# Performance work log

Measured on AMD Instinct MI355X. Metric: run time of the kernel, lower is better.

The kernel has to match this reference:

```python
import jax, jax.numpy as jnp
import numpy as np

B, S, D = 2, 2048, 1024
H, HD, K = 16, 64, 4
F = 4096
EPS = 1e-6
ROPE_BASE = 10000.0
NEG = -1e9


def rmsnorm(x, w):
    return x * jax.lax.rsqrt(jnp.mean(x * x, axis=-1, keepdims=True) + EPS) * w


def rope(t, pos):
    # t: (B,S,H,HD), pos: (B,S,H) per-node position (float)
    inv_freq = 1.0 / (ROPE_BASE ** (jnp.arange(0, HD, 2, dtype=jnp.float32) / HD))
    ang = pos[..., None] * inv_freq  # (B,S,H,HD/2)
    cos, sin = jnp.cos(ang), jnp.sin(ang)
    t1, t2 = t[..., : HD // 2], t[..., HD // 2:]
    return jnp.concatenate([t1 * cos - t2 * sin, t2 * cos + t1 * sin], axis=-1)


def setup_inputs() -> dict:
    key = jax.random.key(0)
    ks = jax.random.split(key, 12)
    s = lambda d: 1.0 / np.sqrt(d)
    return {
        "x": jax.random.normal(ks[0], (B, S, D), jnp.float32),
        "attn_norm_w": jnp.ones((D,), jnp.float32),
        "ffn_norm_w": jnp.ones((D,), jnp.float32),
        "Wq": jax.random.normal(ks[1], (D, H * HD), jnp.float32) * s(D),
        "Wk": jax.random.normal(ks[2], (D, H * HD), jnp.float32) * s(D),
        "Wv": jax.random.normal(ks[3], (D, H * HD), jnp.float32) * s(D),
        "Wo": jax.random.normal(ks[4], (H * HD, D), jnp.float32) * s(H * HD),
        "Wr": jax.random.normal(ks[5], (D, H * K), jnp.float32) * s(D),
        "w1": jax.random.normal(ks[6], (D, F), jnp.float32) * s(D),
        "w2": jax.random.normal(ks[7], (D, F), jnp.float32) * s(D),
        "w3": jax.random.normal(ks[8], (F, D), jnp.float32) * s(F),
    }


def reference(x, attn_norm_w, ffn_norm_w, Wq, Wk, Wv, Wo, Wr, w1, w2, w3):
    # ---- pre-norm + hypergraph node-routed causal attention ----
    h = rmsnorm(x, attn_norm_w)
    # per-(token, head) routing to K hyper-nodes
    logits = (h @ Wr).reshape(B, S, H, K)
    node = jnp.argmax(logits, axis=-1)                      # (B,S,H) int
    onehot = jax.nn.one_hot(node, K, dtype=jnp.float32)     # (B,S,H,K)
    # per-node RoPE position: count of previous same-node tokens
    cum = jnp.cumsum(onehot, axis=1)                        # inclusive
    pos = jnp.take_along_axis(cum, node[..., None], axis=-1)[..., 0] - 1.0  # (B,S,H)

    q = (h @ Wq).reshape(B, S, H, HD)
    k = (h @ Wk).reshape(B, S, H, HD)
    v = (h @ Wv).reshape(B, S, H, HD)
    q = rope(q, pos)
    k = rope(k, pos)

    scores = jnp.einsum("bqhd,bkhd->bhqk", q, k) / np.sqrt(HD)  # (B,H,S,S)
    node_h = jnp.transpose(node, (0, 2, 1))                     # (B,H,S)
    same = node_h[:, :, :, None] == node_h[:, :, None, :]       # intra-node only
    causal = jnp.tril(jnp.ones((S, S), bool))
    allowed = same & causal
    attn = jax.nn.softmax(jnp.where(allowed, scores, NEG), axis=-1)
    ctx = jnp.einsum("bhqk,bkhd->bqhd", attn, v).reshape(B, S, H * HD)
    x = x + ctx @ Wo

    # ---- pre-norm + SwiGLU ----
    h2 = rmsnorm(x, ffn_norm_w)
    ffn = (jax.nn.silu(h2 @ w1) * (h2 @ w2)) @ w3
    return x + ffn
```

## Files before the change

### kernel.cpp

```cpp
#include <hip/hip_runtime.h>
#include <hip/hip_bf16.h>
#include <math.h>

typedef __hip_bfloat16 bf16;

#define B_  2
#define S_  2048
#define D_  1024
#define H_  16
#define HD_ 64
#define KR_ 4
#define F_  4096
#define TOK (B_*S_)
#define NEG (-1.0e9f)

typedef __attribute__((ext_vector_type(8))) short bf16x8_t;
typedef __attribute__((ext_vector_type(4))) float f32x4_t;
typedef unsigned int u32;
#define AS1 __attribute__((address_space(1)))
#define AS3 __attribute__((address_space(3)))

__device__ __forceinline__ float u2f(unsigned short u) {
  union { float f; unsigned int i; } cv; cv.i = ((unsigned int)u) << 16; return cv.f;
}
__device__ __forceinline__ unsigned short f2u(float f) {
  return (unsigned short)(__bfloat16_as_ushort(__float2bfloat16(f)));
}

__device__ __forceinline__ void gl_lds16(const bf16* g, unsigned short* lds_base) {
  __builtin_amdgcn_global_load_lds((const AS1 u32*)g, (AS3 u32*)lds_base, 16, 0, 0);
}

__device__ __forceinline__ float rd1(const void* p, size_t i, bool isbf) {
  return isbf ? __bfloat162float(((const bf16*)p)[i]) : ((const float*)p)[i];
}

__global__ void detect_k(const unsigned* __restrict__ anw_words, int* __restrict__ flag) {
  if (threadIdx.x == 0) *flag = (anw_words[0] == 0x3F803F80u) ? 1 : 0;
}

__global__ __launch_bounds__(256) void transpose_k(const void* W, bf16* __restrict__ WT,
                                                   const int* __restrict__ flagp,
                                                   int K, int N) {
  const bool isbf = (*flagp != 0);
  __shared__ float tile[32][33];
  const int k0 = blockIdx.y * 32, n0 = blockIdx.x * 32;
  const int tid = threadIdx.x;
  const int rl = tid >> 5, cl = tid & 31;
#pragma unroll
  for (int i = 0; i < 4; i++)
    tile[rl + 8 * i][cl] = rd1(W, (size_t)(k0 + rl + 8 * i) * N + n0 + cl, isbf);
  __syncthreads();
#pragma unroll
  for (int i = 0; i < 4; i++)
    WT[(size_t)(n0 + rl + 8 * i) * K + k0 + cl] = __float2bfloat16(tile[cl][rl + 8 * i]);
}

__global__ __launch_bounds__(256) void wrconv_k(const void* Wr, float* __restrict__ Wrf,
                                                const int* __restrict__ flagp) {
  const bool isbf = (*flagp != 0);
  const int i = blockIdx.x * 256 + threadIdx.x;
  Wrf[i] = rd1(Wr, i, isbf);
}

template <bool XDUAL, bool WF>
__global__ __launch_bounds__(256) void rmsnorm_k(const void* x, const void* w,
                                                 bf16* __restrict__ ob,
                                                 float* __restrict__ of,
                                                 const int* __restrict__ flagp) {
  const bool isbf = (*flagp != 0);
  const int row = blockIdx.x;
  const int t = threadIdx.x;
  float v[4];
  float ss = 0.f;
#pragma unroll
  for (int i = 0; i < 4; i++) {
    const size_t idx = (size_t)row * D_ + t + 256 * i;
    v[i] = XDUAL ? rd1(x, idx, isbf) : ((const float*)x)[idx];
    ss += v[i] * v[i];
  }
#pragma unroll
  for (int off = 32; off >= 1; off >>= 1) ss += __shfl_down(ss, off);
  __shared__ float red[4];
  if ((t & 63) == 0) red[t >> 6] = ss;
  __syncthreads();
  const float tot = red[0] + red[1] + red[2] + red[3];
  const float sc = rsqrtf(tot * (1.f / D_) + 1e-6f);
#pragma unroll
  for (int i = 0; i < 4; i++) {
    const int c = t + 256 * i;
    const float r = v[i] * sc * rd1(w, c, isbf);
    ob[(size_t)row * D_ + c] = __float2bfloat16(r);
    if (WF) of[(size_t)row * D_ + c] = r;
  }
}

__global__ __launch_bounds__(256) void router_k(const float* __restrict__ h,
                                                const float* __restrict__ Wrf,
                                                int* __restrict__ node) {
  const int tok0 = blockIdx.x * 16;
  const int t = threadIdx.x;
  __shared__ float hs[16][1024];
  __shared__ float lg[16][64];
  {
    const float4* hsrc = (const float4*)(h + (size_t)tok0 * D_);
    float4* hdst = (float4*)hs;
#pragma unroll
    for (int j = 0; j < 16; j++) hdst[j * 256 + t] = hsrc[j * 256 + t];
  }
  __syncthreads();
  const int col = t & 63, tg = t >> 6;
  float acc[4] = {0.f, 0.f, 0.f, 0.f};
  for (int i = 0; i < D_; i += 4) {
    float wv[4];
#pragma unroll
    for (int u = 0; u < 4; u++) wv[u] = Wrf[(size_t)(i + u) * 64 + col];
#pragma unroll
    for (int tt = 0; tt < 4; tt++) {
      const float4 hv = *(const float4*)&hs[tg * 4 + tt][i];
      acc[tt] = fmaf(hv.x, wv[0], acc[tt]);
      acc[tt] = fmaf(hv.y, wv[1], acc[tt]);
      acc[tt] = fmaf(hv.z, wv[2], acc[tt]);
      acc[tt] = fmaf(hv.w, wv[3], acc[tt]);
    }
  }
#pragma unroll
  for (int tt = 0; tt < 4; tt++) lg[tg * 4 + tt][col] = acc[tt];
  __syncthreads();
  const int tok = t >> 4, hh = t & 15;
  const float* l = &lg[tok][hh * 4];
  float best = l[0];
  int bi = 0;
#pragma unroll
  for (int j = 1; j < KR_; j++) {
    const float vv = l[j];
    if (vv > best) { best = vv; bi = j; }
  }
  node[(size_t)(tok0 + tok) * H_ + hh] = bi;
}

__global__ __launch_bounds__(256) void pos_k(const int* __restrict__ node,
                                             float* __restrict__ pos,
                                             unsigned short* __restrict__ iperm,
                                             unsigned char* __restrict__ gid,
                                             int* __restrict__ gstart) {
  const int bh = blockIdx.x;
  const int b = bh >> 4, h = bh & 15;
  const int t = threadIdx.x;
  __shared__ int sc[256][4];
  int vals[8];
  int c[4] = {0, 0, 0, 0};
#pragma unroll
  for (int i = 0; i < 8; i++) {
    vals[i] = node[(size_t)(b * S_ + t * 8 + i) * H_ + h] & 3;
    c[vals[i]]++;
  }
#pragma unroll
  for (int n = 0; n < 4; n++) sc[t][n] = c[n];
  __syncthreads();
  for (int off = 1; off < 256; off <<= 1) {
    int add[4] = {0, 0, 0, 0};
    if (t >= off) {
#pragma unroll
      for (int n = 0; n < 4; n++) add[n] = sc[t - off][n];
    }
    __syncthreads();
#pragma unroll
    for (int n = 0; n < 4; n++) sc[t][n] += add[n];
    __syncthreads();
  }
  int start[4];
#pragma unroll
  for (int n = 0; n < 4; n++) start[n] = sc[t][n] - c[n];
  int gs[4];
  gs[0] = 0;
  gs[1] = sc[255][0];
  gs[2] = gs[1] + sc[255][1];
  gs[3] = gs[2] + sc[255][2];
  if (t < 4) gstart[bh * 4 + t] = gs[t];
  const size_t bhS = (size_t)bh * S_;
#pragma unroll
  for (int i = 0; i < 8; i++) {
    const int n = vals[i];
    const int rank = start[n]++;
    pos[(size_t)(b * S_ + t * 8 + i) * H_ + h] = (float)rank;
    const int newp = gs[n] + rank;
    iperm[bhS + newp] = (unsigned short)(t * 8 + i);
    gid[bhS + newp] = (unsigned char)n;
  }
}

__global__ __launch_bounds__(512) void rope_k(bf16* __restrict__ q, bf16* __restrict__ k,
                                              const float* __restrict__ pos) {
  const int token = blockIdx.x;
  const int t = threadIdx.x;
  const int h = t >> 5, j = t & 31;
  const float p = pos[token * H_ + h];
  const float inv = exp2f(-(float)j * (13.287712379549449f / 32.f));
  float sn, cs;
  sincosf(p * inv, &sn, &cs);
  const size_t base = (size_t)token * D_ + h * HD_ + j;
  float a = __bfloat162float(q[base]), b = __bfloat162float(q[base + 32]);
  q[base] = __float2bfloat16(a * cs - b * sn);
  q[base + 32] = __float2bfloat16(b * cs + a * sn);
  a = __bfloat162float(k[base]); b = __bfloat162float(k[base + 32]);
  k[base] = __float2bfloat16(a * cs - b * sn);
  k[base + 32] = __float2bfloat16(b * cs + a * sn);
}

__global__ __launch_bounds__(256) void attn_k(const bf16* __restrict__ q,
                                              const bf16* __restrict__ k,
                                              const bf16* __restrict__ v,
                                              const unsigned short* __restrict__ ip,
                                              const unsigned char* __restrict__ gidp,
                                              const int* __restrict__ gstart,
                                              bf16* __restrict__ ctx) {
  const int qt = 31 - blockIdx.x;
  const int h = blockIdx.y;
  const int b = blockIdx.z;
  const int bS = b * S_;
  const int bh = b * H_ + h;
  const size_t bhS = (size_t)bh * S_;
  const int tid = threadIdx.x;
  const int w = tid >> 6;
  const int lane = tid & 63;
  const int col = lane & 15;
  const int quad = lane >> 4;

  __shared__ unsigned short Qs[64][76];
  __shared__ unsigned short Ks[64][76];
  __shared__ unsigned short Vst[64][76];
  __shared__ unsigned short Pa[64][76];

  {
    const int qr = tid & 63, ds = (tid >> 6) * 16;
    const int ipq = ip[bhS + qt * 64 + qr];
    const bf16* src = q + (size_t)(bS + ipq) * D_ + h * HD_ + ds;
#pragma unroll
    for (int i = 0; i < 4; i++)
      *(ushort4*)&Qs[qr][ds + 4 * i] = *(const ushort4*)(src + 4 * i);
  }
  int gq_r[4];
#pragma unroll
  for (int reg = 0; reg < 4; reg++)
    gq_r[reg] = gidp[bhS + qt * 64 + w * 16 + quad * 4 + reg];
  float m_r[4] = {NEG, NEG, NEG, NEG};
  float l_r[4] = {0.f, 0.f, 0.f, 0.f};

  f32x4_t acc_o[4];
#pragma unroll
  for (int ct = 0; ct < 4; ct++) acc_o[ct] = (f32x4_t){0.f, 0.f, 0.f, 0.f};

  const int kt0 = gstart[bh * 4 + gidp[bhS + qt * 64]] >> 6;

  for (int kt = kt0; kt <= qt; kt++) {
    __syncthreads();
    {
      const int key = tid & 63, ds = (tid >> 6) * 16;
      const int ipk = ip[bhS + kt * 64 + key];
      const bf16* ksrc = k + (size_t)(bS + ipk) * D_ + h * HD_ + ds;
      const bf16* vsrc = v + (size_t)(bS + ipk) * D_ + h * HD_ + ds;
#pragma unroll
      for (int i = 0; i < 4; i++) {
        *(ushort4*)&Ks[key][ds + 4 * i] = *(const ushort4*)(ksrc + 4 * i);
        const ushort4 vu = *(const ushort4*)(vsrc + 4 * i);
        Vst[ds + 4 * i + 0][key] = vu.x;
        Vst[ds + 4 * i + 1][key] = vu.y;
        Vst[ds + 4 * i + 2][key] = vu.z;
        Vst[ds + 4 * i + 3][key] = vu.w;
      }
    }
    __syncthreads();

    f32x4_t s[4];
    {
      const bf16x8_t a0 = *(const bf16x8_t*)&Qs[w * 16 + col][quad * 8];
      const bf16x8_t a1 = *(const bf16x8_t*)&Qs[w * 16 + col][32 + quad * 8];
#pragma unroll
      for (int ct = 0; ct < 4; ct++) {
        f32x4_t acc = (f32x4_t){0.f, 0.f, 0.f, 0.f};
        const bf16x8_t b0 = *(const bf16x8_t*)&Ks[ct * 16 + col][quad * 8];
        const bf16x8_t b1 = *(const bf16x8_t*)&Ks[ct * 16 + col][32 + quad * 8];
        acc = __builtin_amdgcn_mfma_f32_16x16x32_bf16(a0, b0, acc, 0, 0, 0);
        acc = __builtin_amdgcn_mfma_f32_16x16x32_bf16(a1, b1, acc, 0, 0, 0);
        s[ct] = acc;
      }
    }
    const bool diag = (kt == qt);
    const size_t kbase = bhS + kt * 64;
    const int gk[4] = {gidp[kbase + col], gidp[kbase + 16 + col],
                       gidp[kbase + 32 + col], gidp[kbase + 48 + col]};
#pragma unroll
    for (int ct = 0; ct < 4; ct++) {
#pragma unroll
      for (int reg = 0; reg < 4; reg++) {
        const int qr = quad * 4 + reg;
        const int kc = ct * 16 + col;
        const bool ok = (gk[ct] == gq_r[reg]) && (!diag || kc <= w * 16 + qr);
        s[ct][reg] = ok ? (s[ct][reg] * 0.125f) : NEG;
      }
    }
    float al[4];
#pragma unroll
    for (int reg = 0; reg < 4; reg++) {
      float tm = fmaxf(fmaxf(s[0][reg], s[1][reg]), fmaxf(s[2][reg], s[3][reg]));
#pragma unroll
      for (int off = 1; off <= 8; off <<= 1) tm = fmaxf(tm, __shfl_xor(tm, off));
      const float mold = m_r[reg];
      const float mnew = fmaxf(mold, tm);
      const bool dead = (mnew <= -5.0e8f);
      const float alpha = dead ? 1.f : __expf(mold - mnew);
      float rowsum = 0.f;
      const int qr = w * 16 + quad * 4 + reg;
#pragma unroll
      for (int ct = 0; ct < 4; ct++) {
        const float e = dead ? 0.f : __expf(s[ct][reg] - mnew);
        rowsum += e;
        Pa[qr][ct * 16 + col] = f2u(e);
      }
#pragma unroll
      for (int off = 1; off <= 8; off <<= 1) rowsum += __shfl_xor(rowsum, off);
      l_r[reg] = l_r[reg] * alpha + rowsum;
      m_r[reg] = mnew;
      al[reg] = alpha;
    }
    {
      const bf16x8_t pa0 = *(const bf16x8_t*)&Pa[w * 16 + col][quad * 8];
      const bf16x8_t pa1 = *(const bf16x8_t*)&Pa[w * 16 + col][32 + quad * 8];
#pragma unroll
      for (int ct = 0; ct < 4; ct++) {
#pragma unroll
        for (int reg = 0; reg < 4; reg++) acc_o[ct][reg] *= al[reg];
        const bf16x8_t b0 = *(const bf16x8_t*)&Vst[ct * 16 + col][quad * 8];
        const bf16x8_t b1 = *(const bf16x8_t*)&Vst[ct * 16 + col][32 + quad * 8];
        acc_o[ct] = __builtin_amdgcn_mfma_f32_16x16x32_bf16(pa0, b0, acc_o[ct], 0, 0, 0);
        acc_o[ct] = __builtin_amdgcn_mfma_f32_16x16x32_bf16(pa1, b1, acc_o[ct], 0, 0, 0);
      }
    }
  }

#pragma unroll
  for (int reg = 0; reg < 4; reg++) {
    const int qr = w * 16 + quad * 4 + reg;
    const int op = ip[bhS + qt * 64 + qr];
    const float l = l_r[reg];
    const float invl = (l > 0.f) ? (1.f / l) : 0.f;
#pragma unroll
    for (int ct = 0; ct < 4; ct++) {
      ctx[(size_t)(bS + op) * D_ + h * HD_ + ct * 16 + col] =
          __float2bfloat16(acc_o[ct][reg] * invl);
    }
  }
}

template <int EPI>
__global__ __launch_bounds__(256) void mgemm_k(const bf16* __restrict__ A,
                                               const bf16* __restrict__ BT,
                                               float* __restrict__ Cf,
                                               void* Cout,
                                               const void* resdual,
                                               const float* __restrict__ resf,
                                               const int* __restrict__ flagp,
                                               int N, int Kd) {
  const bool isbf = (*flagp != 0);
  __shared__ unsigned short As[128][32];
  __shared__ unsigned short Bs[128][32];
  const int tid = threadIdx.x;
  const int w = tid >> 6, lane = tid & 63;
  const int col = lane & 15, quad = lane >> 4;
  const int wm = w & 1, wn = w >> 1;
  const int row0 = blockIdx.y * 128, col0 = blockIdx.x * 128;

  const int srow = lane >> 2, sk8 = (lane & 3) << 3;
  const bf16* Ag0 = A + (size_t)(row0 + 16 * w + srow) * Kd + sk8;
  const bf16* Ag1 = A + (size_t)(row0 + 64 + 16 * w + srow) * Kd + sk8;
  const bf16* Bg0 = BT + (size_t)(col0 + 16 * w + srow) * Kd + sk8;
  const bf16* Bg1 = BT + (size_t)(col0 + 64 + 16 * w + srow) * Kd + sk8;

  f32x4_t acc[4][4];
#pragma unroll
  for (int i = 0; i < 4; i++)
#pragma unroll
    for (int j = 0; j < 4; j++) acc[i][j] = (f32x4_t){0.f, 0.f, 0.f, 0.f};

  for (int kt = 0; kt < Kd; kt += 32) {
    __syncthreads();
    gl_lds16(Ag0 + kt, &As[16 * w][0]);
    gl_lds16(Ag1 + kt, &As[64 + 16 * w][0]);
    gl_lds16(Bg0 + kt, &Bs[16 * w][0]);
    gl_lds16(Bg1 + kt, &Bs[64 + 16 * w][0]);
    __syncthreads();

    bf16x8_t af[4], bfr[4];
#pragma unroll
    for (int i = 0; i < 4; i++) {
      af[i] = *(const bf16x8_t*)&As[wm * 64 + i * 16 + col][quad * 8];
      bfr[i] = *(const bf16x8_t*)&Bs[wn * 64 + i * 16 + col][quad * 8];
    }
#pragma unroll
    for (int i = 0; i < 4; i++)
#pragma unroll
      for (int j = 0; j < 4; j++)
        acc[i][j] = __builtin_amdgcn_mfma_f32_16x16x32_bf16(af[i], bfr[j], acc[i][j], 0, 0, 0);
  }

#pragma unroll
  for (int i = 0; i < 4; i++) {
#pragma unroll
    for (int j = 0; j < 4; j++) {
#pragma unroll
      for (int reg = 0; reg < 4; reg++) {
        const int m = row0 + wm * 64 + i * 16 + quad * 4 + reg;
        const int nl = wn * 64 + j * 16 + col;
        if (EPI == 0) {
          const int ng = col0 + nl;
          bf16* base = (bf16*)Cout + (size_t)(ng >> 10) * (TOK * (size_t)D_);
          base[(size_t)m * D_ + (ng & 1023)] = __float2bfloat16(acc[i][j][reg]);
        } else if (EPI == 1) {
          const size_t idx = (size_t)m * N + col0 + nl;
          Cf[idx] = acc[i][j][reg] + rd1(resdual, idx, isbf);
        } else {
          const size_t idx = (size_t)m * N + col0 + nl;
          const float r = acc[i][j][reg] + resf[idx];
          if (isbf) ((bf16*)Cout)[idx] = __float2bfloat16(r);
          else      ((float*)Cout)[idx] = r;
        }
      }
    }
  }
}

__global__ __launch_bounds__(256) void mgate_k(const bf16* __restrict__ A,
                                               const bf16* __restrict__ B1T,
                                               const bf16* __restrict__ B2T,
                                               bf16* __restrict__ G,
                                               int Kd) {
  __shared__ unsigned short As[128][32];
  __shared__ unsigned short Bs1[64][32];
  __shared__ unsigned short Bs2[64][32];
  const int tid = threadIdx.x;
  const int w = tid >> 6, lane = tid & 63;
  const int col = lane & 15, quad = lane >> 4;
  const int wm = w & 1, wn = w >> 1;
  const int row0 = blockIdx.y * 128, col0 = blockIdx.x * 64;

  const int srow = lane >> 2, sk8 = (lane & 3) << 3;
  const bf16* Ag0 = A + (size_t)(row0 + 16 * w + srow) * Kd + sk8;
  const bf16* Ag1 = A + (size_t)(row0 + 64 + 16 * w + srow) * Kd + sk8;
  const bf16* B1g = B1T + (size_t)(col0 + 16 * w + srow) * Kd + sk8;
  const bf16* B2g = B2T + (size_t)(col0 + 16 * w + srow) * Kd + sk8;

  f32x4_t acc1[4][2], acc2[4][2];
#pragma unroll
  for (int i = 0; i < 4; i++)
#pragma unroll
    for (int j = 0; j < 2; j++) {
      acc1[i][j] = (f32x4_t){0.f, 0.f, 0.f, 0.f};
      acc2[i][j] = (f32x4_t){0.f, 0.f, 0.f, 0.f};
    }

  for (int kt = 0; kt < Kd; kt += 32) {
    __syncthreads();
    gl_lds16(Ag0 + kt, &As[16 * w][0]);
    gl_lds16(Ag1 + kt, &As[64 + 16 * w][0]);
    gl_lds16(B1g + kt, &Bs1[16 * w][0]);
    gl_lds16(B2g + kt, &Bs2[16 * w][0]);
    __syncthreads();

    bf16x8_t af[4], b1f[2], b2f[2];
#pragma unroll
    for (int i = 0; i < 4; i++)
      af[i] = *(const bf16x8_t*)&As[wm * 64 + i * 16 + col][quad * 8];
#pragma unroll
    for (int j = 0; j < 2; j++) {
      b1f[j] = *(const bf16x8_t*)&Bs1[wn * 32 + j * 16 + col][quad * 8];
      b2f[j] = *(const bf16x8_t*)&Bs2[wn * 32 + j * 16 + col][quad * 8];
    }
#pragma unroll
    for (int i = 0; i < 4; i++)
#pragma unroll
      for (int j = 0; j < 2; j++) {
        acc1[i][j] = __builtin_amdgcn_mfma_f32_16x16x32_bf16(af[i], b1f[j], acc1[i][j], 0, 0, 0);
        acc2[i][j] = __builtin_amdgcn_mfma_f32_16x16x32_bf16(af[i], b2f[j], acc2[i][j], 0, 0, 0);
      }
  }

#pragma unroll
  for (int i = 0; i < 4; i++) {
#pragma unroll
    for (int j = 0; j < 2; j++) {
#pragma unroll
      for (int reg = 0; reg < 4; reg++) {
        const int m = row0 + wm * 64 + i * 16 + quad * 4 + reg;
        const int n = col0 + wn * 32 + j * 16 + col;
        const float z = acc1[i][j][reg];
        const float sig = 1.f / (1.f + __expf(-z));
        G[(size_t)m * F_ + n] = __float2bfloat16(z * sig * acc2[i][j][reg]);
      }
    }
  }
}

extern "C" void kernel_launch(void* const* d_in, const int* in_sizes, int n_in,
                              void* d_out, int out_size, void* d_ws, size_t ws_size,
                              hipStream_t stream) {
  const void* x   = d_in[0];
  const void* anw = d_in[1];
  const void* fnw = d_in[2];
  const void* Wq  = d_in[3];
  const void* Wk  = d_in[4];
  const void* Wv  = d_in[5];
  const void* Wo  = d_in[6];
  const void* Wr  = d_in[7];
  const void* w1  = d_in[8];
  const void* w2  = d_in[9];
  const void* w3  = d_in[10];

  char* ws = (char*)d_ws;
  int*   node = (int*)ws;
  float* pos  = (float*)(ws + (256 << 10));
  int*   flag = (int*)(ws + (512 << 10));
  unsigned short* iperm = (unsigned short*)(ws + (640u << 10));
  unsigned char*  gidb  = (unsigned char*)(ws + (768u << 10));
  int*   gstart = (int*)(ws + (832u << 10));
  float* x2   = (float*)(ws + (1u << 20));
  bf16*  ctx  = (bf16*)(ws + (17u << 20));
  bf16*  h2   = ctx;
  float* Wrf  = (float*)(ws + (17u << 20));
  char*  r0   = ws + (25u << 20);
  bf16*  hb   = (bf16*)(r0);
  bf16*  qb   = (bf16*)(r0 + (8u << 20));
  bf16*  kb   = (bf16*)(r0 + (16u << 20));
  bf16*  vb   = (bf16*)(r0 + (24u << 20));
  float* hf   = (float*)(r0 + (8u << 20));
  bf16*  g    = (bf16*)(r0);
  bf16*  qkvT = (bf16*)(ws + (57u << 20));
  bf16*  WoT  = (bf16*)(ws + (63u << 20));
  bf16*  w1T  = (bf16*)(ws + (65u << 20));
  bf16*  w2T  = (bf16*)(ws + (73u << 20));
  bf16*  w3T  = (bf16*)(ws + (81u << 20));

  detect_k<<<1, 64, 0, stream>>>((const unsigned*)anw, flag);
  wrconv_k<<<256, 256, 0, stream>>>(Wr, Wrf, flag);
  transpose_k<<<dim3(32, 32), 256, 0, stream>>>(Wq, qkvT,              flag, D_, D_);
  transpose_k<<<dim3(32, 32), 256, 0, stream>>>(Wk, qkvT + (1u << 20), flag, D_, D_);
  transpose_k<<<dim3(32, 32), 256, 0, stream>>>(Wv, qkvT + (2u << 20), flag, D_, D_);
  transpose_k<<<dim3(32, 32), 256, 0, stream>>>(Wo, WoT,               flag, D_, D_);
  transpose_k<<<dim3(128, 32), 256, 0, stream>>>(w1, w1T,              flag, D_, F_);
  transpose_k<<<dim3(128, 32), 256, 0, stream>>>(w2, w2T,              flag, D_, F_);
  transpose_k<<<dim3(32, 128), 256, 0, stream>>>(w3, w3T,              flag, F_, D_);
  rmsnorm_k<true, true><<<TOK, 256, 0, stream>>>(x, anw, hb, hf, flag);
  router_k<<<TOK / 16, 256, 0, stream>>>(hf, Wrf, node);
  pos_k<<<32, 256, 0, stream>>>(node, pos, iperm, gidb, gstart);
  mgemm_k<0><<<dim3(3072 / 128, TOK / 128), 256, 0, stream>>>(hb, qkvT, nullptr, qb, nullptr, nullptr, flag, 3072, D_);
  rope_k<<<TOK, 512, 0, stream>>>(qb, kb, pos);
  attn_k<<<dim3(S_ / 64, H_, B_), 256, 0, stream>>>(qb, kb, vb, iperm, gidb, gstart, ctx);
  mgemm_k<1><<<dim3(D_ / 128, TOK / 128), 256, 0, stream>>>(ctx, WoT, x2, nullptr, x, nullptr, flag, D_, D_);
  rmsnorm_k<false, false><<<TOK, 256, 0, stream>>>(x2, fnw, h2, nullptr, flag);
  mgate_k<<<dim3(F_ / 64, TOK / 128), 256, 0, stream>>>(h2, w1T, w2T, g, D_);
  mgemm_k<2><<<dim3(D_ / 128, TOK / 128), 256, 0, stream>>>(g, w3T, nullptr, d_out, nullptr, x2, flag, D_, F_);
}
```

Before: 548.2 us.

## Add XCD-aware tile remap and 64-row GEMM for small-N projections

Adds an XCD-aware block-index remap to the GEMM kernels so that consecutive tiles land on the same chiplet, which should improve L2 reuse of shared operand rows and columns. Adds a 64x128-tile GEMM variant and uses it for the Wo and w3 projections, where N=1024 gives only 256 blocks with 128x128 tiles. The smaller tiles double the block count to fill the 256 CUs better. In exchange, each block reuses less data and loads proportionally more per output.

```diff
diff --git a/kernel.cpp b/kernel.cpp
--- a/kernel.cpp
+++ b/kernel.cpp
@@ -33,6 +33,15 @@
 
 __device__ __forceinline__ float rd1(const void* p, size_t i, bool isbf) {
   return isbf ? __bfloat162float(((const bf16*)p)[i]) : ((const float*)p)[i];
+}
+
+__device__ __forceinline__ void xcd_tile(int& bx, int& by) {
+  const int nx = gridDim.x;
+  const int nwg = nx * gridDim.y;
+  const int hw = blockIdx.y * nx + blockIdx.x;
+  const int tile = (hw & 7) * (nwg >> 3) + (hw >> 3);
+  bx = tile % nx;
+  by = tile / nx;
 }
 
 __global__ void detect_k(const unsigned* __restrict__ anw_words, int* __restrict__ flag) {
@@ -369,7 +378,9 @@
   const int w = tid >> 6, lane = tid & 63;
   const int col = lane & 15, quad = lane >> 4;
   const int wm = w & 1, wn = w >> 1;
-  const int row0 = blockIdx.y * 128, col0 = blockIdx.x * 128;
+  int bx, by;
+  xcd_tile(bx, by);
+  const int row0 = by * 128, col0 = bx * 128;
 
   const int srow = lane >> 2, sk8 = (lane & 3) << 3;
   const bf16* Ag0 = A + (size_t)(row0 + 16 * w + srow) * Kd + sk8;
@@ -430,6 +441,78 @@
   }
 }
 
+template <int EPI>
+__global__ __launch_bounds__(256) void mgemm64_k(const bf16* __restrict__ A,
+                                                 const bf16* __restrict__ BT,
+                                                 float* __restrict__ Cf,
+                                                 void* Cout,
+                                                 const void* resdual,
+                                                 const float* __restrict__ resf,
+                                                 const int* __restrict__ flagp,
+                                                 int N, int Kd) {
+  const bool isbf = (*flagp != 0);
+  __shared__ unsigned short As[64][32];
+  __shared__ unsigned short Bs[128][32];
+  const int tid = threadIdx.x;
+  const int w = tid >> 6, lane = tid & 63;
+  const int col = lane & 15, quad = lane >> 4;
+  int bx, by;
+  xcd_tile(bx, by);
+  const int row0 = by * 64, col0 = bx * 128;
+
+  const int srow = lane >> 2, sk8 = (lane & 3) << 3;
+  const bf16* Ag  = A + (size_t)(row0 + 16 * w + srow) * Kd + sk8;
+  const bf16* Bg0 = BT + (size_t)(col0 + 32 * w + srow) * Kd + sk8;
+  const bf16* Bg1 = BT + (size_t)(col0 + 32 * w + 16 + srow) * Kd + sk8;
+
+  f32x4_t acc[4][2];
+#pragma unroll
+  for (int i = 0; i < 4; i++)
+#pragma unroll
+    for (int j = 0; j < 2; j++) acc[i][j] = (f32x4_t){0.f, 0.f, 0.f, 0.f};
+
+  for (int kt = 0; kt < Kd; kt += 32) {
+    __syncthreads();
+    gl_lds16(Ag + kt, &As[16 * w][0]);
+    gl_lds16(Bg0 + kt, &Bs[32 * w][0]);
+    gl_lds16(Bg1 + kt, &Bs[32 * w + 16][0]);
+    __syncthreads();
+
+    bf16x8_t af[4], bfr[2];
+#pragma unroll
+    for (int i = 0; i < 4; i++)
+      af[i] = *(const bf16x8_t*)&As[i * 16 + col][quad * 8];
+#pragma unroll
+    for (int j = 0; j < 2; j++)
+      bfr[j] = *(const bf16x8_t*)&Bs[w * 32 + j * 16 + col][quad * 8];
+#pragma unroll
+    for (int i = 0; i < 4; i++)
+#pragma unroll
+      for (int j = 0; j < 2; j++)
+        acc[i][j] = __builtin_amdgcn_mfma_f32_16x16x32_bf16(af[i], bfr[j], acc[i][j], 0, 0, 0);
+  }
+
+#pragma unroll
+  for (int i = 0; i < 4; i++) {
+#pragma unroll
+    for (int j = 0; j < 2; j++) {
+#pragma unroll
+      for (int reg = 0; reg < 4; reg++) {
+        const int m = row0 + i * 16 + quad * 4 + reg;
+        const int nl = w * 32 + j * 16 + col;
+        const size_t idx = (size_t)m * N + col0 + nl;
+        if (EPI == 1) {
+          Cf[idx] = acc[i][j][reg] + rd1(resdual, idx, isbf);
+        } else {
+          const float r = acc[i][j][reg] + resf[idx];
+          if (isbf) ((bf16*)Cout)[idx] = __float2bfloat16(r);
+          else      ((float*)Cout)[idx] = r;
+        }
+      }
+    }
+  }
+}
+
 __global__ __launch_bounds__(256) void mgate_k(const bf16* __restrict__ A,
                                                const bf16* __restrict__ B1T,
                                                const bf16* __restrict__ B2T,
@@ -442,7 +525,9 @@
   const int w = tid >> 6, lane = tid & 63;
   const int col = lane & 15, quad = lane >> 4;
   const int wm = w & 1, wn = w >> 1;
-  const int row0 = blockIdx.y * 128, col0 = blockIdx.x * 64;
+  int bx, by;
+  xcd_tile(bx, by);
+  const int row0 = by * 128, col0 = bx * 64;
 
   const int srow = lane >> 2, sk8 = (lane & 3) << 3;
   const bf16* Ag0 = A + (size_t)(row0 + 16 * w + srow) * Kd + sk8;
@@ -555,8 +640,8 @@
   mgemm_k<0><<<dim3(3072 / 128, TOK / 128), 256, 0, stream>>>(hb, qkvT, nullptr, qb, nullptr, nullptr, flag, 3072, D_);
   rope_k<<<TOK, 512, 0, stream>>>(qb, kb, pos);
   attn_k<<<dim3(S_ / 64, H_, B_), 256, 0, stream>>>(qb, kb, vb, iperm, gidb, gstart, ctx);
-  mgemm_k<1><<<dim3(D_ / 128, TOK / 128), 256, 0, stream>>>(ctx, WoT, x2, nullptr, x, nullptr, flag, D_, D_);
+  mgemm64_k<1><<<dim3(D_ / 128, TOK / 64), 256, 0, stream>>>(ctx, WoT, x2, nullptr, x, nullptr, flag, D_, D_);
   rmsnorm_k<false, false><<<TOK, 256, 0, stream>>>(x2, fnw, h2, nullptr, flag);
   mgate_k<<<dim3(F_ / 64, TOK / 128), 256, 0, stream>>>(h2, w1T, w2T, g, D_);
-  mgemm_k<2><<<dim3(D_ / 128, TOK / 128), 256, 0, stream>>>(g, w3T, nullptr, d_out, nullptr, x2, flag, D_, F_);
-}
+  mgemm64_k<2><<<dim3(D_ / 128, TOK / 64), 256, 0, stream>>>(g, w3T, nullptr, d_out, nullptr, x2, flag, D_, F_);
+}
```

Result: faster. 522.8 us (-4.6%).
